# Kernel tuning notes

Hardware: AMD Instinct MI355X
Metric: run time of the kernel (lower is better)

## Reference

```python
import jax, jax.numpy as jnp
import numpy as np

NEG_INF = -1e30  # stand-in for -inf that is safe under fp16/bf16


def setup_inputs() -> dict:
    key = jax.random.key(0)
    k1, k2, k3, k4, k5 = jax.random.split(key, 5)
    B, NC, H, Wd = 32, 256, 64, 64
    MW, E = 32, 768
    images = jax.random.normal(k1, (B, NC, H, Wd), dtype=jnp.float32)
    words = jax.random.normal(k2, (B, MW, E), dtype=jnp.float32)
    # mask: True where word is ignored; ensure at least one word is attended per row
    mask = jax.random.randint(k3, (B, MW), 0, 2).astype(bool)
    mask = mask.at[:, 0].set(False)
    W = jax.random.normal(k4, (NC, E), dtype=jnp.float32) * (1.0 / np.sqrt(E))
    b = jax.random.normal(k5, (NC,), dtype=jnp.float32) * 0.01
    return {"images": images, "words": words, "mask": mask, "W": W, "b": b}


def reference(images, words, mask, W, b):
    B, NC, H, Wd = images.shape
    _, MW, E = words.shape
    # 1x1 conv over words == linear projection emb_dim -> nc_in
    # words_p: [B, nc_in, max_words]
    words_p = jnp.einsum('bme,ce->bcm', words, W) + b[None, :, None]
    # images flattened to pixels: [B, h*w, nc_in]
    imgs = images.reshape(B, NC, H * Wd).transpose(0, 2, 1)
    # attention scores: [B, h*w, max_words], scaled by 1/sqrt(nc_in)
    attn = jnp.einsum('bpc,bcm->bpm', imgs, words_p) * (1.0 / np.sqrt(NC))
    attn = jnp.where(mask[:, None, :], NEG_INF, attn)
    attn = jax.nn.softmax(attn, axis=-1)
    # weighted word sum per pixel: [B, nc_in, h*w]
    weighted = jnp.einsum('bcm,bpm->bcp', words_p, attn)
    weighted_words = weighted.reshape(B, NC, H, Wd)
    attn_out = attn.transpose(0, 2, 1).reshape(B, MW, H, Wd)
    return weighted_words, attn_out
```

## Files before the change

kernel.cpp:

```cpp
#include <hip/hip_runtime.h>
#include <math.h>

#define B_   32
#define NC_  256
#define HW_  4096
#define MW_  32
#define E_   768
#define NEG_BIG -3.0e38f

typedef float vf2 __attribute__((ext_vector_type(2)));
typedef float vf4 __attribute__((ext_vector_type(4)));

#define PART_OFF   0
#define WT_OFF     2359296
#define WORDST_OFF 2555904

__global__ __launch_bounds__(256) void prep_kernel(
    const float* __restrict__ W, const float* __restrict__ words,
    float* __restrict__ WT, float* __restrict__ wordsT) {
  const int tid = threadIdx.x;
  const int tx = tid & 31, ty = tid >> 5;
  if (blockIdx.x < 192) {
    __shared__ float t[32][33];
    const int tc = blockIdx.x / 24, te = blockIdx.x % 24;
    const int c0 = tc * 32, e0 = te * 32;
#pragma unroll
    for (int k = 0; k < 4; ++k) {
      const int r = ty + 8 * k;
      t[r][tx] = W[(c0 + r) * E_ + e0 + tx];
    }
    __syncthreads();
#pragma unroll
    for (int k = 0; k < 4; ++k) {
      const int r = ty + 8 * k;
      WT[(e0 + r) * NC_ + c0 + tx] = t[tx][r];
    }
  } else {
    __shared__ float t[32][33];
    const int idx = blockIdx.x - 192;
    const int b = idx / 24, te = idx % 24;
    const int e0 = te * 32;
    const float* wsrc = words + (size_t)b * MW_ * E_;
    float* wdst = wordsT + (size_t)b * E_ * MW_;
#pragma unroll
    for (int k = 0; k < 4; ++k) {
      const int m = ty + 8 * k;
      t[m][tx] = wsrc[m * E_ + e0 + tx];
    }
    __syncthreads();
#pragma unroll
    for (int k = 0; k < 4; ++k) {
      const int e = ty + 8 * k;
      wdst[(e0 + e) * MW_ + tx] = t[tx][e];
    }
  }
}

__global__ __launch_bounds__(256) void stage1_partial(
    const float* __restrict__ wordsT, const float* __restrict__ WT,
    float* __restrict__ part) {
  const int c = threadIdx.x;
  const int b = blockIdx.x >> 3;
  const int chunk = blockIdx.x & 7;
  const int e0 = chunk * 96;
  const float* wt = wordsT + (size_t)b * E_ * MW_;
  float acc[32];
#pragma unroll
  for (int m = 0; m < 32; ++m) acc[m] = 0.f;
#pragma unroll 2
  for (int e = e0; e < e0 + 96; ++e) {
    const float wv = WT[(size_t)e * NC_ + c];
    const float* wr = wt + e * MW_;
#pragma unroll
    for (int m = 0; m < 32; ++m) acc[m] = fmaf(wv, wr[m], acc[m]);
  }
  float* pp = part + ((size_t)chunk * 32 + b) * 32 * 256;
#pragma unroll
  for (int m = 0; m < 32; ++m) pp[m * 256 + c] = acc[m];
}

__global__ __launch_bounds__(128) void attention_fused(
    const float* __restrict__ images, const float* __restrict__ part,
    const float* __restrict__ bias, const void* __restrict__ mask_raw,
    float* __restrict__ out_w, float* __restrict__ out_a) {
  __shared__ float lwp[NC_ * MW_];
  __shared__ int is_word;
  const int tid = threadIdx.x;
  const int b = blockIdx.x & 31;
  const int po = ((blockIdx.x >> 5) << 7) + tid;
  const vf2* imgb = (const vf2*)(images + (size_t)b * NC_ * HW_);

  if (tid == 0) is_word = 1;

  vf2 cur[8];
#pragma unroll
  for (int j = 0; j < 8; ++j)
    cur[j] = __builtin_nontemporal_load(&imgb[((size_t)j << 11) + po]);

#pragma unroll
  for (int half = 0; half < 2; ++half) {
    const int c = (half << 7) + tid;
    const float bc = bias[c];
    float row[32];
#pragma unroll
    for (int m = 0; m < 32; ++m) row[m] = bc;
#pragma unroll
    for (int k = 0; k < 8; ++k) {
      const float* pk = part + (((size_t)k * 32 + b) * 32) * 256 + c;
#pragma unroll
      for (int m = 0; m < 32; ++m) row[m] += pk[(size_t)m * 256];
    }
    vf4* dst = (vf4*)(lwp + (c << 5));
#pragma unroll
    for (int q = 0; q < 8; ++q) {
      vf4 t;
      t.x = row[4 * q]; t.y = row[4 * q + 1];
      t.z = row[4 * q + 2]; t.w = row[4 * q + 3];
      dst[q] = t;
    }
  }
  __syncthreads();

  {
    const int* mi = (const int*)mask_raw;
#pragma unroll
    for (int q = 0; q < 2; ++q) {
      const int v = mi[q * 128 + tid];
      if (v != 0 && v != 1 && v != 0x3F800000) is_word = 0;
    }
  }
  __syncthreads();
  unsigned mbits = 0;
  if (is_word) {
    const int* mi = (const int*)mask_raw;
#pragma unroll
    for (int m = 0; m < 32; ++m)
      mbits |= (mi[(b << 5) + m] != 0 ? 1u : 0u) << m;
  } else {
    const unsigned char* mb = (const unsigned char*)mask_raw;
#pragma unroll
    for (int m = 0; m < 32; ++m)
      mbits |= (mb[(b << 5) + m] != 0 ? 1u : 0u) << m;
  }

  float s0[32], s1[32];
#pragma unroll
  for (int m = 0; m < 32; ++m) { s0[m] = 0.f; s1[m] = 0.f; }

  vf4 wa[8], wb[8];
#pragma unroll
  for (int q = 0; q < 8; ++q) wa[q] = ((const vf4*)lwp)[q];

#pragma unroll 1
  for (int c0 = 0; c0 < 256; c0 += 8) {
    vf2 nxt[8];
    if (c0 + 8 < 256) {
#pragma unroll
      for (int j = 0; j < 8; ++j)
        nxt[j] = __builtin_nontemporal_load(&imgb[((size_t)(c0 + 8 + j) << 11) + po]);
    }
#pragma unroll
    for (int j = 0; j < 8; ++j) {
      const int cn = c0 + j + 1;
      if ((j & 1) == 0) {
        if (cn < 256) {
#pragma unroll
          for (int q = 0; q < 8; ++q) wb[q] = ((const vf4*)lwp)[(cn << 3) + q];
        }
        const float* wr = (const float*)wa;
        const vf2 v = cur[j];
#pragma unroll
        for (int m = 0; m < 32; ++m) {
          s0[m] = fmaf(v.x, wr[m], s0[m]);
          s1[m] = fmaf(v.y, wr[m], s1[m]);
        }
      } else {
        if (cn < 256) {
#pragma unroll
          for (int q = 0; q < 8; ++q) wa[q] = ((const vf4*)lwp)[(cn << 3) + q];
        }
        const float* wr = (const float*)wb;
        const vf2 v = cur[j];
#pragma unroll
        for (int m = 0; m < 32; ++m) {
          s0[m] = fmaf(v.x, wr[m], s0[m]);
          s1[m] = fmaf(v.y, wr[m], s1[m]);
        }
      }
    }
#pragma unroll
    for (int j = 0; j < 8; ++j) cur[j] = nxt[j];
  }

  float mx0 = NEG_BIG, mx1 = NEG_BIG;
#pragma unroll
  for (int m = 0; m < 32; ++m) {
    s0[m] *= 0.0625f;
    s1[m] *= 0.0625f;
    if (!((mbits >> m) & 1u)) {
      mx0 = fmaxf(mx0, s0[m]);
      mx1 = fmaxf(mx1, s1[m]);
    }
  }
  float sum0 = 0.f, sum1 = 0.f;
#pragma unroll
  for (int m = 0; m < 32; ++m) {
    const bool msk = (mbits >> m) & 1u;
    const float e0 = msk ? 0.f : __expf(s0[m] - mx0);
    const float e1 = msk ? 0.f : __expf(s1[m] - mx1);
    s0[m] = e0; s1[m] = e1;
    sum0 += e0; sum1 += e1;
  }
  const float inv0 = 1.f / sum0, inv1 = 1.f / sum1;
  vf2* oa = (vf2*)out_a;
#pragma unroll
  for (int m = 0; m < 32; ++m) {
    s0[m] *= inv0;
    s1[m] *= inv1;
    vf2 a; a.x = s0[m]; a.y = s1[m];
    __builtin_nontemporal_store(a, &oa[((size_t)((b << 5) + m) << 11) + po]);
  }

  vf2* ow = (vf2*)out_w;
#pragma unroll
  for (int q = 0; q < 8; ++q) wa[q] = ((const vf4*)lwp)[q];

#pragma unroll 1
  for (int c0 = 0; c0 < 256; c0 += 8) {
#pragma unroll
    for (int j = 0; j < 8; ++j) {
      const int c = c0 + j;
      const int cn = c + 1;
      float o0 = 0.f, o1 = 0.f;
      if ((j & 1) == 0) {
        if (cn < 256) {
#pragma unroll
          for (int q = 0; q < 8; ++q) wb[q] = ((const vf4*)lwp)[(cn << 3) + q];
        }
        const float* wr = (const float*)wa;
#pragma unroll
        for (int m = 0; m < 32; ++m) {
          o0 = fmaf(wr[m], s0[m], o0);
          o1 = fmaf(wr[m], s1[m], o1);
        }
      } else {
        if (cn < 256) {
#pragma unroll
          for (int q = 0; q < 8; ++q) wa[q] = ((const vf4*)lwp)[(cn << 3) + q];
        }
        const float* wr = (const float*)wb;
#pragma unroll
        for (int m = 0; m < 32; ++m) {
          o0 = fmaf(wr[m], s0[m], o0);
          o1 = fmaf(wr[m], s1[m], o1);
        }
      }
      vf2 o; o.x = o0; o.y = o1;
      __builtin_nontemporal_store(o, &ow[((size_t)((b << 8) + c) << 11) + po]);
    }
  }
}

extern "C" void kernel_launch(void* const* d_in, const int* in_sizes, int n_in,
                              void* d_out, int out_size, void* d_ws, size_t ws_size,
                              hipStream_t stream) {
  const float* images = (const float*)d_in[0];
  const float* words  = (const float*)d_in[1];
  const void*  mask   = d_in[2];
  const float* W      = (const float*)d_in[3];
  const float* bias   = (const float*)d_in[4];

  float* ws     = (float*)d_ws;
  float* part   = ws + PART_OFF;
  float* WT     = ws + WT_OFF;
  float* wordsT = ws + WORDST_OFF;

  float* out_w = (float*)d_out;
  float* out_a = out_w + (size_t)B_ * NC_ * HW_;

  prep_kernel<<<960, 256, 0, stream>>>(W, words, WT, wordsT);
  stage1_partial<<<256, 256, 0, stream>>>(wordsT, WT, part);
  attention_fused<<<512, 128, 0, stream>>>(images, part, bias, mask, out_w, out_a);
}
```

Baseline: 318.6 us.

## Process four pixels per thread in attention kernel and halve grid

Each thread of the fused attention kernel now handles four pixels (vf4 loads and stores) instead of two, so every LDS word-projection read is reused across four accumulators. The grid drops to 256 blocks, and launch bounds ask for one block per SM to free registers. The explicit wa/wb register double-buffering of projection rows is replaced by direct LDS reads, and the LDS fill is rewritten to write vf4 with a different thread mapping. The risks are very high register pressure (128 score registers per thread, possible spills) and only 256 blocks on a 256-CU part, which leaves little latency hiding.

```diff
diff --git a/kernel.cpp b/kernel.cpp
--- a/kernel.cpp
+++ b/kernel.cpp
@@ -79,7 +79,7 @@
   for (int m = 0; m < 32; ++m) pp[m * 256 + c] = acc[m];
 }
 
-__global__ __launch_bounds__(128) void attention_fused(
+__global__ __launch_bounds__(128, 1) void attention_fused(
     const float* __restrict__ images, const float* __restrict__ part,
     const float* __restrict__ bias, const void* __restrict__ mask_raw,
     float* __restrict__ out_w, float* __restrict__ out_a) {
@@ -88,35 +88,35 @@
   const int tid = threadIdx.x;
   const int b = blockIdx.x & 31;
   const int po = ((blockIdx.x >> 5) << 7) + tid;
-  const vf2* imgb = (const vf2*)(images + (size_t)b * NC_ * HW_);
+  const vf4* imgb = (const vf4*)(images + (size_t)b * NC_ * HW_);
 
   if (tid == 0) is_word = 1;
 
-  vf2 cur[8];
+  vf4 cur[8];
 #pragma unroll
   for (int j = 0; j < 8; ++j)
-    cur[j] = __builtin_nontemporal_load(&imgb[((size_t)j << 11) + po]);
-
-#pragma unroll
-  for (int half = 0; half < 2; ++half) {
-    const int c = (half << 7) + tid;
-    const float bc = bias[c];
-    float row[32];
-#pragma unroll
-    for (int m = 0; m < 32; ++m) row[m] = bc;
-#pragma unroll
-    for (int k = 0; k < 8; ++k) {
-      const float* pk = part + (((size_t)k * 32 + b) * 32) * 256 + c;
-#pragma unroll
-      for (int m = 0; m < 32; ++m) row[m] += pk[(size_t)m * 256];
-    }
-    vf4* dst = (vf4*)(lwp + (c << 5));
-#pragma unroll
-    for (int q = 0; q < 8; ++q) {
-      vf4 t;
-      t.x = row[4 * q]; t.y = row[4 * q + 1];
-      t.z = row[4 * q + 2]; t.w = row[4 * q + 3];
-      dst[q] = t;
+    cur[j] = __builtin_nontemporal_load(&imgb[((size_t)j << 10) + po]);
+
+  {
+    vf4* dst = (vf4*)lwp;
+#pragma unroll
+    for (int k2 = 0; k2 < 16; ++k2) {
+      const int v = tid + (k2 << 7);
+      const int c = v >> 3;
+      const int mq = v & 7;
+      const float bc = bias[c];
+      float v0 = bc, v1 = bc, v2 = bc, v3 = bc;
+#pragma unroll
+      for (int pk = 0; pk < 8; ++pk) {
+        const float* pp = part + (((size_t)pk * 32 + b) * 32) * 256;
+        const int mb = mq << 2;
+        v0 += pp[(mb + 0) * 256 + c];
+        v1 += pp[(mb + 1) * 256 + c];
+        v2 += pp[(mb + 2) * 256 + c];
+        v3 += pp[(mb + 3) * 256 + c];
+      }
+      vf4 t; t.x = v0; t.y = v1; t.z = v2; t.w = v3;
+      dst[v] = t;
     }
   }
   __syncthreads();
@@ -143,120 +143,81 @@
       mbits |= (mb[(b << 5) + m] != 0 ? 1u : 0u) << m;
   }
 
-  float s0[32], s1[32];
-#pragma unroll
-  for (int m = 0; m < 32; ++m) { s0[m] = 0.f; s1[m] = 0.f; }
-
-  vf4 wa[8], wb[8];
-#pragma unroll
-  for (int q = 0; q < 8; ++q) wa[q] = ((const vf4*)lwp)[q];
+  float s0[32], s1[32], s2[32], s3[32];
+#pragma unroll
+  for (int m = 0; m < 32; ++m) { s0[m] = 0.f; s1[m] = 0.f; s2[m] = 0.f; s3[m] = 0.f; }
 
 #pragma unroll 1
   for (int c0 = 0; c0 < 256; c0 += 8) {
-    vf2 nxt[8];
+    vf4 nxt[8];
     if (c0 + 8 < 256) {
 #pragma unroll
       for (int j = 0; j < 8; ++j)
-        nxt[j] = __builtin_nontemporal_load(&imgb[((size_t)(c0 + 8 + j) << 11) + po]);
+        nxt[j] = __builtin_nontemporal_load(&imgb[((size_t)(c0 + 8 + j) << 10) + po]);
     }
 #pragma unroll
     for (int j = 0; j < 8; ++j) {
-      const int cn = c0 + j + 1;
-      if ((j & 1) == 0) {
-        if (cn < 256) {
-#pragma unroll
-          for (int q = 0; q < 8; ++q) wb[q] = ((const vf4*)lwp)[(cn << 3) + q];
-        }
-        const float* wr = (const float*)wa;
-        const vf2 v = cur[j];
-#pragma unroll
-        for (int m = 0; m < 32; ++m) {
-          s0[m] = fmaf(v.x, wr[m], s0[m]);
-          s1[m] = fmaf(v.y, wr[m], s1[m]);
-        }
-      } else {
-        if (cn < 256) {
-#pragma unroll
-          for (int q = 0; q < 8; ++q) wa[q] = ((const vf4*)lwp)[(cn << 3) + q];
-        }
-        const float* wr = (const float*)wb;
-        const vf2 v = cur[j];
-#pragma unroll
-        for (int m = 0; m < 32; ++m) {
-          s0[m] = fmaf(v.x, wr[m], s0[m]);
-          s1[m] = fmaf(v.y, wr[m], s1[m]);
-        }
+      const float* wr = lwp + ((c0 + j) << 5);
+      const vf4 v = cur[j];
+#pragma unroll
+      for (int m = 0; m < 32; ++m) {
+        s0[m] = fmaf(v.x, wr[m], s0[m]);
+        s1[m] = fmaf(v.y, wr[m], s1[m]);
+        s2[m] = fmaf(v.z, wr[m], s2[m]);
+        s3[m] = fmaf(v.w, wr[m], s3[m]);
       }
     }
 #pragma unroll
     for (int j = 0; j < 8; ++j) cur[j] = nxt[j];
   }
 
-  float mx0 = NEG_BIG, mx1 = NEG_BIG;
+  float mx0 = NEG_BIG, mx1 = NEG_BIG, mx2 = NEG_BIG, mx3 = NEG_BIG;
 #pragma unroll
   for (int m = 0; m < 32; ++m) {
-    s0[m] *= 0.0625f;
-    s1[m] *= 0.0625f;
+    s0[m] *= 0.0625f; s1[m] *= 0.0625f; s2[m] *= 0.0625f; s3[m] *= 0.0625f;
     if (!((mbits >> m) & 1u)) {
-      mx0 = fmaxf(mx0, s0[m]);
-      mx1 = fmaxf(mx1, s1[m]);
-    }
-  }
-  float sum0 = 0.f, sum1 = 0.f;
+      mx0 = fmaxf(mx0, s0[m]); mx1 = fmaxf(mx1, s1[m]);
+      mx2 = fmaxf(mx2, s2[m]); mx3 = fmaxf(mx3, s3[m]);
+    }
+  }
+  float sum0 = 0.f, sum1 = 0.f, sum2 = 0.f, sum3 = 0.f;
 #pragma unroll
   for (int m = 0; m < 32; ++m) {
     const bool msk = (mbits >> m) & 1u;
     const float e0 = msk ? 0.f : __expf(s0[m] - mx0);
     const float e1 = msk ? 0.f : __expf(s1[m] - mx1);
-    s0[m] = e0; s1[m] = e1;
-    sum0 += e0; sum1 += e1;
+    const float e2 = msk ? 0.f : __expf(s2[m] - mx2);
+    const float e3 = msk ? 0.f : __expf(s3[m] - mx3);
+    s0[m] = e0; s1[m] = e1; s2[m] = e2; s3[m] = e3;
+    sum0 += e0; sum1 += e1; sum2 += e2; sum3 += e3;
   }
   const float inv0 = 1.f / sum0, inv1 = 1.f / sum1;
-  vf2* oa = (vf2*)out_a;
+  const float inv2 = 1.f / sum2, inv3 = 1.f / sum3;
+  vf4* oa = (vf4*)out_a;
 #pragma unroll
   for (int m = 0; m < 32; ++m) {
-    s0[m] *= inv0;
-    s1[m] *= inv1;
-    vf2 a; a.x = s0[m]; a.y = s1[m];
-    __builtin_nontemporal_store(a, &oa[((size_t)((b << 5) + m) << 11) + po]);
-  }
-
-  vf2* ow = (vf2*)out_w;
-#pragma unroll
-  for (int q = 0; q < 8; ++q) wa[q] = ((const vf4*)lwp)[q];
-
+    s0[m] *= inv0; s1[m] *= inv1; s2[m] *= inv2; s3[m] *= inv3;
+    vf4 a; a.x = s0[m]; a.y = s1[m]; a.z = s2[m]; a.w = s3[m];
+    __builtin_nontemporal_store(a, &oa[((size_t)((b << 5) + m) << 10) + po]);
+  }
+
+  vf4* ow = (vf4*)out_w;
 #pragma unroll 1
   for (int c0 = 0; c0 < 256; c0 += 8) {
 #pragma unroll
     for (int j = 0; j < 8; ++j) {
       const int c = c0 + j;
-      const int cn = c + 1;
-      float o0 = 0.f, o1 = 0.f;
-      if ((j & 1) == 0) {
-        if (cn < 256) {
-#pragma unroll
-          for (int q = 0; q < 8; ++q) wb[q] = ((const vf4*)lwp)[(cn << 3) + q];
-        }
-        const float* wr = (const float*)wa;
-#pragma unroll
-        for (int m = 0; m < 32; ++m) {
-          o0 = fmaf(wr[m], s0[m], o0);
-          o1 = fmaf(wr[m], s1[m], o1);
-        }
-      } else {
-        if (cn < 256) {
-#pragma unroll
-          for (int q = 0; q < 8; ++q) wa[q] = ((const vf4*)lwp)[(cn << 3) + q];
-        }
-        const float* wr = (const float*)wb;
-#pragma unroll
-        for (int m = 0; m < 32; ++m) {
-          o0 = fmaf(wr[m], s0[m], o0);
-          o1 = fmaf(wr[m], s1[m], o1);
-        }
+      const float* wr = lwp + (c << 5);
+      float o0 = 0.f, o1 = 0.f, o2 = 0.f, o3 = 0.f;
+#pragma unroll
+      for (int m = 0; m < 32; ++m) {
+        o0 = fmaf(wr[m], s0[m], o0);
+        o1 = fmaf(wr[m], s1[m], o1);
+        o2 = fmaf(wr[m], s2[m], o2);
+        o3 = fmaf(wr[m], s3[m], o3);
       }
-      vf2 o; o.x = o0; o.y = o1;
-      __builtin_nontemporal_store(o, &ow[((size_t)((b << 8) + c) << 11) + po]);
+      vf4 o; o.x = o0; o.y = o1; o.z = o2; o.w = o3;
+      __builtin_nontemporal_store(o, &ow[((size_t)((b << 8) + c) << 10) + po]);
     }
   }
 }
@@ -280,5 +241,5 @@
 
   prep_kernel<<<960, 256, 0, stream>>>(W, words, WT, wordsT);
   stage1_partial<<<256, 256, 0, stream>>>(wordsT, WT, part);
-  attention_fused<<<512, 128, 0, stream>>>(images, part, bias, mask, out_w, out_a);
-}
+  attention_fused<<<256, 128, 0, stream>>>(images, part, bias, mask, out_w, out_a);
+}
```

Result: slower. 362.2 us (+13.7%).
